# Kernel tuning notes

Hardware: AMD Instinct MI355X
Metric: run time of the kernel (lower is better)

The kernel has to match this reference:

```python
import jax, jax.numpy as jnp
import numpy as np

B, IN_C, OUT_C, K, S_IN, S_OUT = 16, 32, 32, 14, 9, 9
EPS = 1e-8


def setup_inputs() -> dict:
    key = jax.random.key(0)
    k1, k2, k3 = jax.random.split(key, 3)
    x = jax.random.normal(k1, (B, IN_C, K, K, S_IN), dtype=jnp.float32)
    p = jax.random.uniform(k2, (B, IN_C, K, K), dtype=jnp.float32)
    # learned parameter: (1, in_c, out_c, k, k, s_out, s_in)
    T = jax.random.normal(k3, (1, IN_C, OUT_C, K, K, S_OUT, S_IN), dtype=jnp.float32)
    return {"x": x, "p": p, "epoch": 0, "T": T}


def reference(x, p, epoch, T):
    b, c, h, w, s_in = x.shape
    Ts = T[0] * 0.1  # (c, o, h, w, s_out, s_in)
    o, t = Ts.shape[1], Ts.shape[4]
    # per-location tiny matmul: (s_out,s_in) @ (s_in,) broadcast over b,c,o,h,w
    # output laid out as (b, c, h, w, o, t) matching permute(0,1,3,4,2,5)
    pred = jnp.einsum('cohwts,bchws->bchwot', Ts, x)
    pred = pred.reshape(b, c * h * w, o, t)          # (b, N, out_c, s_out)
    pf = p.reshape(b, c * h * w, 1, 1)               # (b, N, 1, 1)
    psum = pf.sum(axis=1)                            # (b, 1, 1)
    caps = (pred * pf).sum(axis=1) / (psum + EPS)    # (b, out_c, s_out)
    diff = pred - caps[:, None]                      # (b, N, out_c, s_out)
    var = (diff ** 2 * pf).sum(axis=1) / (psum + EPS)  # (b, out_c, s_out)
    vs = var.sum(axis=2)                             # (b, out_c)
    p_updated = 1.0 - vs / (vs.max(axis=1, keepdims=True) + EPS)
    return caps, p_updated
```

## Files before the change

kernel.cpp:

```cpp
#include <hip/hip_runtime.h>

#define EPSF 1e-8f

constexpr int B_  = 16;
constexpr int C_  = 32;
constexpr int O_  = 32;
constexpr int HW  = 196;
constexpr int T9  = 9;
constexpr int CH  = 28;
constexpr int ROWF = 12;
constexpr int CHUNK_F4 = CH * 81 / 4;
constexpr int LDSF = CH * T9 * ROWF;
constexpr int KSPL = 2;
constexpr int PART_W = C_ * KSPL;
constexpr int PART_N = B_ * O_ * T9 * PART_W;
constexpr int XT_N = C_ * B_ * 9 * HW;
constexpr int PT_N = C_ * B_ * HW;

__global__ __launch_bounds__(256) void caps_pre(
    const float* __restrict__ x, const float* __restrict__ p,
    float* __restrict__ xT, float* __restrict__ pT)
{
    const int idx = blockIdx.x * 256 + threadIdx.x;
    const int stride = gridDim.x * 256;
    for (int m = idx; m < XT_N; m += stride) {
        const int hw = m % HW;
        const int r  = m / HW;
        const int s  = r % 9;
        const int r2 = r / 9;
        const int b  = r2 % B_;
        const int c  = r2 / B_;
        xT[m] = 0.1f * x[((size_t)(b * C_ + c) * HW + hw) * 9 + s];
    }
    for (int m = idx; m < PT_N; m += stride) {
        const int hw = m % HW;
        const int r2 = m / HW;
        const int b  = r2 % B_;
        const int c  = r2 / B_;
        pT[m] = p[(size_t)(b * C_ + c) * HW + hw];
    }
}

__global__ __launch_bounds__(256) void caps_main(
    const float* __restrict__ T,
    const float* __restrict__ xT, const float* __restrict__ pT,
    float* __restrict__ part1,
    float* __restrict__ part2)
{
    const int o   = blockIdx.x;
    const int c   = blockIdx.y;
    const int z   = blockIdx.z;
    const int tid = threadIdx.x;
    const int b   = tid >> 4;
    const int r   = tid & 15;

    const int k0 = z * 4;
    const int k1 = (z == 0) ? 4 : 7;

    __shared__ float tsh[LDSF];

    const float* Tb = T + (size_t)(c * O_ + o) * (HW * 81);
    const float* xb = xT + (size_t)(c * B_ + b) * 9 * HW;
    const float* pb = pT + (size_t)(c * B_ + b) * HW;

    float acc1[9], acc2[9];
#pragma unroll
    for (int t = 0; t < 9; ++t) { acc1[t] = 0.f; acc2[t] = 0.f; }

    for (int k = k0; k < k1; ++k) {
        if (k != k0) __syncthreads();

        const float4* g4 = (const float4*)(Tb + (size_t)k * CH * 81);
#pragma unroll
        for (int q = 0; q < 3; ++q) {
            const int i = tid + q * 256;
            if (i < CHUNK_F4) {
                const float4 v = g4[i];
                const int e = i * 4;
#pragma unroll
                for (int k2 = 0; k2 < 4; ++k2) {
                    const int e2 = e + k2;
                    tsh[e2 + 3 * (e2 / 9)] = ((const float*)&v)[k2];
                }
            }
        }
        __syncthreads();

#pragma unroll
        for (int rep = 0; rep < 2; ++rep) {
            const int row = rep * 16 + r;
            if (row < CH) {
                const int hw = k * CH + row;
                float xr[9];
#pragma unroll
                for (int s = 0; s < 9; ++s) xr[s] = xb[(size_t)s * HW + hw];
                const float pf = pb[hw];
                const float* rowb = tsh + row * (T9 * ROWF);
#pragma unroll
                for (int t = 0; t < 9; ++t) {
                    const float4 ta = *(const float4*)(rowb + t * ROWF);
                    const float4 tb = *(const float4*)(rowb + t * ROWF + 4);
                    const float t8  = rowb[t * ROWF + 8];
                    float pr = ta.x * xr[0];
                    pr = fmaf(ta.y, xr[1], pr);
                    pr = fmaf(ta.z, xr[2], pr);
                    pr = fmaf(ta.w, xr[3], pr);
                    pr = fmaf(tb.x, xr[4], pr);
                    pr = fmaf(tb.y, xr[5], pr);
                    pr = fmaf(tb.z, xr[6], pr);
                    pr = fmaf(tb.w, xr[7], pr);
                    pr = fmaf(t8,   xr[8], pr);
                    const float q1 = pf * pr;
                    acc1[t] += q1;
                    acc2[t] = fmaf(q1, pr, acc2[t]);
                }
            }
        }
    }

#pragma unroll
    for (int t = 0; t < 9; ++t) {
        float v1 = acc1[t], v2 = acc2[t];
#pragma unroll
        for (int m = 1; m < 16; m <<= 1) {
            v1 += __shfl_xor(v1, m, 64);
            v2 += __shfl_xor(v2, m, 64);
        }
        if (r == 0) {
            const size_t base = ((size_t)(b * O_ + o) * 9 + t) * PART_W + c * KSPL + z;
            part1[base] = v1;
            part2[base] = v2;
        }
    }
}

__global__ __launch_bounds__(256) void caps_final(
    const float* __restrict__ p,
    const float* __restrict__ part1, const float* __restrict__ part2,
    float* __restrict__ out)
{
    const int b   = blockIdx.x;
    const int tid = threadIdx.x;

    __shared__ float vlds[O_ * T9];
    __shared__ float red[4];
    __shared__ float s_psum;

    const float* pb = p + (size_t)b * (C_ * HW);
    float a = 0.f;
    for (int i = tid; i < C_ * HW; i += 256) a += pb[i];
#pragma unroll
    for (int m = 1; m < 64; m <<= 1) a += __shfl_xor(a, m, 64);
    if ((tid & 63) == 0) red[tid >> 6] = a;
    __syncthreads();
    if (tid == 0) s_psum = (red[0] + red[1]) + (red[2] + red[3]);
    __syncthreads();
    const float psum  = s_psum;
    const float denom = psum + EPSF;

    for (int e = tid; e < O_ * T9; e += 256) {
        const float4* q1 = (const float4*)(part1 + (size_t)(b * 288 + e) * PART_W);
        const float4* q2 = (const float4*)(part2 + (size_t)(b * 288 + e) * PART_W);
        float s1 = 0.f, s2 = 0.f;
#pragma unroll
        for (int i = 0; i < PART_W / 4; ++i) {
            const float4 v1 = q1[i], v2 = q2[i];
            s1 += (v1.x + v1.y) + (v1.z + v1.w);
            s2 += (v2.x + v2.y) + (v2.z + v2.w);
        }
        const float caps = s1 / denom;
        out[(size_t)b * 288 + e] = caps;
        vlds[e] = (s2 - 2.f * caps * s1 + caps * caps * psum) / denom;
    }
    __syncthreads();

    if (tid < O_) {
        float vs = 0.f;
#pragma unroll
        for (int t = 0; t < 9; ++t) vs += vlds[tid * 9 + t];
        float mx = vs;
#pragma unroll
        for (int msk = 1; msk < 32; msk <<= 1) mx = fmaxf(mx, __shfl_xor(mx, msk, 32));
        out[(size_t)B_ * O_ * T9 + b * O_ + tid] = 1.f - vs / (mx + EPSF);
    }
}

extern "C" void kernel_launch(void* const* d_in, const int* in_sizes, int n_in,
                              void* d_out, int out_size, void* d_ws, size_t ws_size,
                              hipStream_t stream)
{
    (void)in_sizes; (void)n_in; (void)out_size; (void)ws_size;
    const float* x = (const float*)d_in[0];
    const float* p = (const float*)d_in[1];
    const float* T = (const float*)d_in[3];
    float* out = (float*)d_out;

    float* part1 = (float*)d_ws;
    float* part2 = part1 + PART_N;
    float* xT    = part2 + PART_N;
    float* pT    = xT + XT_N;

    caps_pre<<<1024, 256, 0, stream>>>(x, p, xT, pT);
    dim3 gridA(O_, C_, KSPL);
    caps_main<<<gridA, 256, 0, stream>>>(T, xT, pT, part1, part2);
    caps_final<<<B_, 256, 0, stream>>>(p, part1, part2, out);
}
```

Baseline: 57.88 us.

## Remap caps_main so each thread handles four batches and collapse second-moment accumulator

```diff
diff --git a/kernel.cpp b/kernel.cpp
--- a/kernel.cpp
+++ b/kernel.cpp
@@ -7,13 +7,13 @@
 constexpr int O_  = 32;
 constexpr int HW  = 196;
 constexpr int T9  = 9;
-constexpr int CH  = 28;
+constexpr int CH  = 64;
 constexpr int ROWF = 12;
-constexpr int CHUNK_F4 = CH * 81 / 4;
 constexpr int LDSF = CH * T9 * ROWF;
 constexpr int KSPL = 2;
-constexpr int PART_W = C_ * KSPL;
-constexpr int PART_N = B_ * O_ * T9 * PART_W;
+constexpr int PW  = C_ * KSPL;
+constexpr int P1_N = B_ * O_ * T9 * PW;
+constexpr int P2_N = B_ * O_ * PW;
 constexpr int XT_N = C_ * B_ * 9 * HW;
 constexpr int PT_N = C_ * B_ * HW;
 
@@ -45,104 +45,112 @@
     const float* __restrict__ T,
     const float* __restrict__ xT, const float* __restrict__ pT,
     float* __restrict__ part1,
-    float* __restrict__ part2)
-{
-    const int o   = blockIdx.x;
-    const int c   = blockIdx.y;
-    const int z   = blockIdx.z;
-    const int tid = threadIdx.x;
-    const int b   = tid >> 4;
-    const int r   = tid & 15;
-
-    const int k0 = z * 4;
-    const int k1 = (z == 0) ? 4 : 7;
+    float* __restrict__ part2s)
+{
+    const int o    = blockIdx.x;
+    const int c    = blockIdx.y;
+    const int z    = blockIdx.z;
+    const int tid  = threadIdx.x;
+    const int bg   = tid >> 6;
+    const int lane = tid & 63;
 
     __shared__ float tsh[LDSF];
 
     const float* Tb = T + (size_t)(c * O_ + o) * (HW * 81);
-    const float* xb = xT + (size_t)(c * B_ + b) * 9 * HW;
-    const float* pb = pT + (size_t)(c * B_ + b) * HW;
-
-    float acc1[9], acc2[9];
-#pragma unroll
-    for (int t = 0; t < 9; ++t) { acc1[t] = 0.f; acc2[t] = 0.f; }
-
-    for (int k = k0; k < k1; ++k) {
+
+    float acc1[4][9];
+    float a2s[4];
+#pragma unroll
+    for (int j = 0; j < 4; ++j) {
+        a2s[j] = 0.f;
+#pragma unroll
+        for (int t = 0; t < 9; ++t) acc1[j][t] = 0.f;
+    }
+
+    const int k0 = z * 2;
+    for (int k = k0; k < k0 + 2; ++k) {
+        const int hw0 = k * CH;
+        const int R   = (HW - hw0 < CH) ? (HW - hw0) : CH;
         if (k != k0) __syncthreads();
 
-        const float4* g4 = (const float4*)(Tb + (size_t)k * CH * 81);
-#pragma unroll
-        for (int q = 0; q < 3; ++q) {
-            const int i = tid + q * 256;
-            if (i < CHUNK_F4) {
-                const float4 v = g4[i];
-                const int e = i * 4;
-#pragma unroll
-                for (int k2 = 0; k2 < 4; ++k2) {
-                    const int e2 = e + k2;
-                    tsh[e2 + 3 * (e2 / 9)] = ((const float*)&v)[k2];
+        const int nf4 = (R * 81) >> 2;
+        const float4* g4 = (const float4*)(Tb + (size_t)hw0 * 81);
+        for (int i = tid; i < nf4; i += 256) {
+            const float4 v = g4[i];
+            const int e = i * 4;
+#pragma unroll
+            for (int k2 = 0; k2 < 4; ++k2) {
+                const int e2 = e + k2;
+                tsh[e2 + 3 * (e2 / 9)] = ((const float*)&v)[k2];
+            }
+        }
+        __syncthreads();
+
+        if (lane < R) {
+            const int hw = hw0 + lane;
+            float xr[4][9], pw[4];
+#pragma unroll
+            for (int j = 0; j < 4; ++j) {
+                const int b = bg * 4 + j;
+                const float* xg = xT + (size_t)(c * B_ + b) * 9 * HW + hw;
+#pragma unroll
+                for (int s = 0; s < 9; ++s) xr[j][s] = xg[(size_t)s * HW];
+                pw[j] = pT[(size_t)(c * B_ + b) * HW + hw];
+            }
+            const float* rowb = tsh + lane * (T9 * ROWF);
+#pragma unroll
+            for (int t = 0; t < 9; ++t) {
+                const float4 ta  = *(const float4*)(rowb + t * ROWF);
+                const float4 tb4 = *(const float4*)(rowb + t * ROWF + 4);
+                const float t8   = rowb[t * ROWF + 8];
+#pragma unroll
+                for (int j = 0; j < 4; ++j) {
+                    float pr = ta.x * xr[j][0];
+                    pr = fmaf(ta.y,  xr[j][1], pr);
+                    pr = fmaf(ta.z,  xr[j][2], pr);
+                    pr = fmaf(ta.w,  xr[j][3], pr);
+                    pr = fmaf(tb4.x, xr[j][4], pr);
+                    pr = fmaf(tb4.y, xr[j][5], pr);
+                    pr = fmaf(tb4.z, xr[j][6], pr);
+                    pr = fmaf(tb4.w, xr[j][7], pr);
+                    pr = fmaf(t8,    xr[j][8], pr);
+                    const float q1 = pw[j] * pr;
+                    acc1[j][t] += q1;
+                    a2s[j] = fmaf(q1, pr, a2s[j]);
                 }
             }
         }
-        __syncthreads();
-
-#pragma unroll
-        for (int rep = 0; rep < 2; ++rep) {
-            const int row = rep * 16 + r;
-            if (row < CH) {
-                const int hw = k * CH + row;
-                float xr[9];
-#pragma unroll
-                for (int s = 0; s < 9; ++s) xr[s] = xb[(size_t)s * HW + hw];
-                const float pf = pb[hw];
-                const float* rowb = tsh + row * (T9 * ROWF);
-#pragma unroll
-                for (int t = 0; t < 9; ++t) {
-                    const float4 ta = *(const float4*)(rowb + t * ROWF);
-                    const float4 tb = *(const float4*)(rowb + t * ROWF + 4);
-                    const float t8  = rowb[t * ROWF + 8];
-                    float pr = ta.x * xr[0];
-                    pr = fmaf(ta.y, xr[1], pr);
-                    pr = fmaf(ta.z, xr[2], pr);
-                    pr = fmaf(ta.w, xr[3], pr);
-                    pr = fmaf(tb.x, xr[4], pr);
-                    pr = fmaf(tb.y, xr[5], pr);
-                    pr = fmaf(tb.z, xr[6], pr);
-                    pr = fmaf(tb.w, xr[7], pr);
-                    pr = fmaf(t8,   xr[8], pr);
-                    const float q1 = pf * pr;
-                    acc1[t] += q1;
-                    acc2[t] = fmaf(q1, pr, acc2[t]);
-                }
-            }
-        }
-    }
-
-#pragma unroll
-    for (int t = 0; t < 9; ++t) {
-        float v1 = acc1[t], v2 = acc2[t];
-#pragma unroll
-        for (int m = 1; m < 16; m <<= 1) {
-            v1 += __shfl_xor(v1, m, 64);
-            v2 += __shfl_xor(v2, m, 64);
-        }
-        if (r == 0) {
-            const size_t base = ((size_t)(b * O_ + o) * 9 + t) * PART_W + c * KSPL + z;
-            part1[base] = v1;
-            part2[base] = v2;
-        }
+    }
+
+#pragma unroll
+    for (int j = 0; j < 4; ++j) {
+        const int b = bg * 4 + j;
+#pragma unroll
+        for (int t = 0; t < 9; ++t) {
+            float v = acc1[j][t];
+#pragma unroll
+            for (int m = 1; m < 64; m <<= 1) v += __shfl_xor(v, m, 64);
+            if (lane == 0)
+                part1[((size_t)(b * O_ + o) * 9 + t) * PW + c * KSPL + z] = v;
+        }
+        float v2 = a2s[j];
+#pragma unroll
+        for (int m = 1; m < 64; m <<= 1) v2 += __shfl_xor(v2, m, 64);
+        if (lane == 0)
+            part2s[(size_t)(b * O_ + o) * PW + c * KSPL + z] = v2;
     }
 }
 
 __global__ __launch_bounds__(256) void caps_final(
     const float* __restrict__ p,
-    const float* __restrict__ part1, const float* __restrict__ part2,
+    const float* __restrict__ part1, const float* __restrict__ part2s,
     float* __restrict__ out)
 {
     const int b   = blockIdx.x;
     const int tid = threadIdx.x;
 
-    __shared__ float vlds[O_ * T9];
+    __shared__ float w1[O_ * T9];
+    __shared__ float w2[O_ * T9];
     __shared__ float red[4];
     __shared__ float s_psum;
 
@@ -159,29 +167,37 @@
     const float denom = psum + EPSF;
 
     for (int e = tid; e < O_ * T9; e += 256) {
-        const float4* q1 = (const float4*)(part1 + (size_t)(b * 288 + e) * PART_W);
-        const float4* q2 = (const float4*)(part2 + (size_t)(b * 288 + e) * PART_W);
-        float s1 = 0.f, s2 = 0.f;
-#pragma unroll
-        for (int i = 0; i < PART_W / 4; ++i) {
-            const float4 v1 = q1[i], v2 = q2[i];
-            s1 += (v1.x + v1.y) + (v1.z + v1.w);
-            s2 += (v2.x + v2.y) + (v2.z + v2.w);
+        const float4* q1 = (const float4*)(part1 + (size_t)(b * 288 + e) * PW);
+        float s1 = 0.f;
+#pragma unroll
+        for (int i = 0; i < PW / 4; ++i) {
+            const float4 v = q1[i];
+            s1 += (v.x + v.y) + (v.z + v.w);
         }
         const float caps = s1 / denom;
         out[(size_t)b * 288 + e] = caps;
-        vlds[e] = (s2 - 2.f * caps * s1 + caps * caps * psum) / denom;
+        w1[e] = caps * s1;
+        w2[e] = caps * caps;
     }
     __syncthreads();
 
     if (tid < O_) {
-        float vs = 0.f;
-#pragma unroll
-        for (int t = 0; t < 9; ++t) vs += vlds[tid * 9 + t];
+        const int o = tid;
+        const float4* q2 = (const float4*)(part2s + (size_t)(b * O_ + o) * PW);
+        float s2 = 0.f;
+#pragma unroll
+        for (int i = 0; i < PW / 4; ++i) {
+            const float4 v = q2[i];
+            s2 += (v.x + v.y) + (v.z + v.w);
+        }
+        float d2 = 0.f, dc = 0.f;
+#pragma unroll
+        for (int t = 0; t < 9; ++t) { d2 += w1[o * 9 + t]; dc += w2[o * 9 + t]; }
+        float vs = (s2 - 2.f * d2 + psum * dc) / denom;
         float mx = vs;
 #pragma unroll
         for (int msk = 1; msk < 32; msk <<= 1) mx = fmaxf(mx, __shfl_xor(mx, msk, 32));
-        out[(size_t)B_ * O_ * T9 + b * O_ + tid] = 1.f - vs / (mx + EPSF);
+        out[(size_t)B_ * O_ * T9 + b * O_ + o] = 1.f - vs / (mx + EPSF);
     }
 }
 
@@ -195,13 +211,13 @@
     const float* T = (const float*)d_in[3];
     float* out = (float*)d_out;
 
-    float* part1 = (float*)d_ws;
-    float* part2 = part1 + PART_N;
-    float* xT    = part2 + PART_N;
-    float* pT    = xT + XT_N;
+    float* part1  = (float*)d_ws;
+    float* part2s = part1 + P1_N;
+    float* xT     = part2s + P2_N;
+    float* pT     = xT + XT_N;
 
     caps_pre<<<1024, 256, 0, stream>>>(x, p, xT, pT);
     dim3 gridA(O_, C_, KSPL);
-    caps_main<<<gridA, 256, 0, stream>>>(T, xT, pT, part1, part2);
-    caps_final<<<B_, 256, 0, stream>>>(p, part1, part2, out);
-}
+    caps_main<<<gridA, 256, 0, stream>>>(T, xT, pT, part1, part2s);
+    caps_final<<<B_, 256, 0, stream>>>(p, part1, part2s, out);
+}
```

New measurement: 83.96 us. 1.45x slower.
